# Performance work log

Hardware: AMD Instinct MI355X
Metric: run time of the kernel (lower is better)

## Reference

```python
import jax, jax.numpy as jnp
import numpy as np

N = 50000          # num nodes
E = 800000         # num edges (avg degree 16)
H = 8              # num_heads
CH = [64, 64, 64, 32]  # [in_features] + conv_channels
EPS = 1e-5


def setup_inputs() -> dict:
    key = jax.random.key(0)
    ks = jax.random.split(key, 20)
    x = jax.random.normal(ks[0], (N, CH[0]), jnp.float32)
    src = jax.random.randint(ks[1], (E,), 0, N, dtype=jnp.int32)
    dst = jax.random.randint(ks[2], (E,), 0, N, dtype=jnp.int32)
    dst = jnp.where(src == dst, (dst + 1) % N, dst)  # no self-loops (remove_self_loops)
    edge_index = jnp.stack([src, dst])  # [2, E]

    def lin(k, shape):
        return jax.random.uniform(k, shape, jnp.float32) * 0.1

    inp = {"x": x, "edge_index": edge_index}
    ki = 3
    for layer, (cin, cout) in enumerate(zip(CH[:-1], CH[1:]), start=1):
        inp[f"W{layer}"] = lin(ks[ki], (H * cout, cin)); ki += 1
        inp[f"U{layer}"] = lin(ks[ki], (H, cin)); ki += 1
        inp[f"c{layer}"] = jax.random.normal(ks[ki], (H,), jnp.float32) * 0.1; ki += 1
        inp[f"b{layer}"] = jax.random.normal(ks[ki], (cout,), jnp.float32) * 0.1; ki += 1
        if layer < 3:  # batch norm on intermediate layers only
            inp[f"g{layer}"] = jnp.ones((cout,), jnp.float32)
            inp[f"be{layer}"] = jnp.zeros((cout,), jnp.float32)
    return inp


def _conv(x, src, dst, inv_count, W, U, c, b, out_ch):
    # FeatureSteeredConvolution (translation-invariant attention), mean aggr.
    xi = x[dst]                                   # [E2, Cin] target features
    xj = x[src]                                   # [E2, Cin] source features
    attn = jax.nn.softmax((xi - xj) @ U.T + c, axis=1)   # [E2, H]
    proj = (xj @ W.T).reshape(-1, H, out_ch)      # [E2, H, Cout]
    msg = jnp.einsum('eh,eho->eo', attn, proj)    # [E2, Cout]
    agg = jax.ops.segment_sum(msg, dst, num_segments=N) * inv_count[:, None]
    return agg + b


def _bn(x, g, be):
    # BatchNorm1d, training mode (batch stats, biased variance)
    m = x.mean(axis=0)
    v = ((x - m) ** 2).mean(axis=0)
    return g * (x - m) * jax.lax.rsqrt(v + EPS) + be


def reference(x, edge_index, W1, U1, c1, b1, g1, be1,
              W2, U2, c2, b2, g2, be2, W3, U3, c3, b3):
    loops = jnp.arange(N, dtype=edge_index.dtype)
    src = jnp.concatenate([edge_index[0], loops])  # add_self_loops
    dst = jnp.concatenate([edge_index[1], loops])
    count = jax.ops.segment_sum(jnp.ones_like(dst, jnp.float32), dst, num_segments=N)
    inv_count = 1.0 / count  # every node has its self-loop, so count >= 1

    h = _conv(x, src, dst, inv_count, W1, U1, c1, b1, CH[1])
    h = _bn(jax.nn.relu(h), g1, be1)
    h = _conv(h, src, dst, inv_count, W2, U2, c2, b2, CH[2])
    h = _bn(jax.nn.relu(h), g2, be2)
    return _conv(h, src, dst, inv_count, W3, U3, c3, b3, CH[3])
```

## Files before the change

kernel.cpp:

```cpp
#include <hip/hip_runtime.h>
#include <hip/hip_bf16.h>
#include <hip/hip_fp16.h>
#include <math.h>

constexpr int NN = 50000;
constexpr int NE = 800000;
constexpr float L2E = 1.44269504f;
constexpr int SBLK = 256;
constexpr int SGRID = (NN + SBLK - 1) / SBLK;

typedef __attribute__((ext_vector_type(8))) short bf16x8;
typedef __attribute__((ext_vector_type(4))) float f32x4;

__device__ inline float b2f(unsigned short u) {
  union { unsigned int i; float f; } v;
  v.i = ((unsigned int)u) << 16;
  return v.f;
}

__global__ void k_deg(const int* __restrict__ dst, int* __restrict__ degin) {
  int i = blockIdx.x * blockDim.x + threadIdx.x;
  if (i < NE) atomicAdd(&degin[dst[i]], 1);
}

__global__ void k_inv(const int* __restrict__ degin, float* __restrict__ inv) {
  int i = blockIdx.x * blockDim.x + threadIdx.x;
  if (i < NN) inv[i] = 1.0f / (float)(degin[i] + 1);
}

__global__ void k_scan1(const int* __restrict__ deg, int* __restrict__ bsum) {
  int i = blockIdx.x * SBLK + threadIdx.x;
  int v = (i < NN) ? deg[i] : 0;
#pragma unroll
  for (int off = 32; off; off >>= 1) v += __shfl_down(v, off, 64);
  __shared__ int ws[SBLK / 64];
  if ((threadIdx.x & 63) == 0) ws[threadIdx.x >> 6] = v;
  __syncthreads();
  if (threadIdx.x == 0) {
    int s = 0;
#pragma unroll
    for (int w = 0; w < SBLK / 64; ++w) s += ws[w];
    bsum[blockIdx.x] = s;
  }
}

__global__ void k_scan2(int* __restrict__ bsum) {
  __shared__ int ls[256];
  int t = threadIdx.x;
  int v = (t < SGRID) ? bsum[t] : 0;
  ls[t] = v;
  __syncthreads();
  for (int off = 1; off < 256; off <<= 1) {
    int u = (t >= off) ? ls[t - off] : 0;
    __syncthreads();
    ls[t] += u;
    __syncthreads();
  }
  if (t < SGRID) bsum[t] = ls[t] - v;
}

__global__ void k_scan3(const int* __restrict__ deg, const int* __restrict__ bsum,
                        int* __restrict__ base, int* __restrict__ cursor) {
  __shared__ int ls[SBLK];
  int t = threadIdx.x;
  int i = blockIdx.x * SBLK + t;
  int v = (i < NN) ? deg[i] : 0;
  ls[t] = v;
  __syncthreads();
  for (int off = 1; off < SBLK; off <<= 1) {
    int u = (t >= off) ? ls[t - off] : 0;
    __syncthreads();
    ls[t] += u;
    __syncthreads();
  }
  int ex = ls[t] - v + bsum[blockIdx.x];
  if (i < NN) { base[i] = ex; cursor[i] = ex; }
}

__global__ void k_scatter(const int* __restrict__ src, const int* __restrict__ dst,
                          int* __restrict__ cursor, int* __restrict__ csrc) {
  int e = blockIdx.x * blockDim.x + threadIdx.x;
  if (e < NE) {
    int pos = atomicAdd(&cursor[dst[e]], 1);
    csrc[pos] = src[e];
  }
}

__global__ void k_dstpos(const int* __restrict__ cscbase, const int* __restrict__ degin,
                         int* __restrict__ dstpos) {
  const int lane = threadIdx.x & 63;
  const int n = (int)(((long)blockIdx.x * blockDim.x + threadIdx.x) >> 6);
  if (n >= NN) return;
  const int base = cscbase[n];
  const int end = base + degin[n];
  for (int k = base + lane; k < end; k += 64) dstpos[k] = n;
}

__global__ void k_f2b(const float* __restrict__ in, __hip_bfloat16* __restrict__ out,
                      long n4) {
  long i = (long)blockIdx.x * blockDim.x + threadIdx.x;
  if (i >= n4) return;
  float4 v = reinterpret_cast<const float4*>(in)[i];
  ushort4 o;
  o.x = __hip_bfloat16_raw(__float2bfloat16(v.x)).x;
  o.y = __hip_bfloat16_raw(__float2bfloat16(v.y)).x;
  o.z = __hip_bfloat16_raw(__float2bfloat16(v.z)).x;
  o.w = __hip_bfloat16_raw(__float2bfloat16(v.w)).x;
  reinterpret_cast<ushort4*>(out)[i] = o;
}

__global__ void k_wt(const float* __restrict__ w1, const float* __restrict__ w2,
                     const float* __restrict__ w3, __hip_bfloat16* __restrict__ t1,
                     __hip_bfloat16* __restrict__ t2, __hip_bfloat16* __restrict__ t3) {
  int i = blockIdx.x * blockDim.x + threadIdx.x;
  const int n1 = 64 * 512, n2 = 64 * 512, n3 = 32 * 512;
  const float* w; __hip_bfloat16* t; int cout; int j = i;
  if (j < n1) { w = w1; t = t1; cout = 64; }
  else if ((j -= n1) < n2) { w = w2; t = t2; cout = 64; }
  else if ((j -= n2) < n3) { w = w3; t = t3; cout = 32; }
  else return;
  int o = j >> 9;
  int hc = j & 511;
  int h = hc >> 6, c = hc & 63;
  t[j] = __float2bfloat16(w[(h * cout + o) * 64 + c]);
}

__global__ void k_q(const float* __restrict__ X, const float* __restrict__ U,
                    float* __restrict__ q) {
  int n = blockIdx.x * blockDim.x + threadIdx.x;
  if (n >= NN) return;
  float4 xr[16];
  const float4* X4 = reinterpret_cast<const float4*>(X) + (size_t)n * 16;
#pragma unroll
  for (int i = 0; i < 16; ++i) xr[i] = X4[i];
  const float4* U4 = reinterpret_cast<const float4*>(U);
#pragma unroll
  for (int h = 0; h < 8; ++h) {
    float a = 0.f;
#pragma unroll
    for (int i = 0; i < 16; ++i) {
      float4 u = U4[h * 16 + i];
      a = fmaf(xr[i].x, u.x, a);
      a = fmaf(xr[i].y, u.y, a);
      a = fmaf(xr[i].z, u.z, a);
      a = fmaf(xr[i].w, u.w, a);
    }
    q[(size_t)n * 8 + h] = a * L2E;
  }
}

__global__ void k_attn(const int* __restrict__ csrc, const int* __restrict__ dstpos,
                       const float* __restrict__ q, const float* __restrict__ cvec,
                       const float* __restrict__ inv, uint4* __restrict__ a) {
  int k = blockIdx.x * blockDim.x + threadIdx.x;
  if (k >= NE) return;
  int s = csrc[k], d = dstpos[k];

  const float4* q4 = reinterpret_cast<const float4*>(q);
  const float4* c4 = reinterpret_cast<const float4*>(cvec);
  float4 qd0 = q4[2 * d], qd1 = q4[2 * d + 1];
  float4 qs0 = q4[2 * s], qs1 = q4[2 * s + 1];
  float4 c0 = c4[0], c1 = c4[1];

  float e[8];
  e[0] = __builtin_amdgcn_exp2f(qd0.x - qs0.x + c0.x * L2E);
  e[1] = __builtin_amdgcn_exp2f(qd0.y - qs0.y + c0.y * L2E);
  e[2] = __builtin_amdgcn_exp2f(qd0.z - qs0.z + c0.z * L2E);
  e[3] = __builtin_amdgcn_exp2f(qd0.w - qs0.w + c0.w * L2E);
  e[4] = __builtin_amdgcn_exp2f(qd1.x - qs1.x + c1.x * L2E);
  e[5] = __builtin_amdgcn_exp2f(qd1.y - qs1.y + c1.y * L2E);
  e[6] = __builtin_amdgcn_exp2f(qd1.z - qs1.z + c1.z * L2E);
  e[7] = __builtin_amdgcn_exp2f(qd1.w - qs1.w + c1.w * L2E);

  float sum = ((e[0] + e[1]) + (e[2] + e[3])) + ((e[4] + e[5]) + (e[6] + e[7]));
  float r = __builtin_amdgcn_rcpf(sum) * inv[d];

  __half2 h0 = __floats2half2_rn(e[0] * r, e[1] * r);
  __half2 h1 = __floats2half2_rn(e[2] * r, e[3] * r);
  __half2 h2 = __floats2half2_rn(e[4] * r, e[5] * r);
  __half2 h3 = __floats2half2_rn(e[6] * r, e[7] * r);
  uint4 o;
  o.x = *(unsigned int*)&h0;
  o.y = *(unsigned int*)&h1;
  o.z = *(unsigned int*)&h2;
  o.w = *(unsigned int*)&h3;
  a[k] = o;
}

#define ZACC(AV, XS)                                                      \
  do {                                                                    \
    float2 f0 = __half22float2(*(__half2*)&(AV).x);                       \
    float2 f1 = __half22float2(*(__half2*)&(AV).y);                       \
    float2 f2 = __half22float2(*(__half2*)&(AV).z);                       \
    float2 f3 = __half22float2(*(__half2*)&(AV).w);                       \
    z[0] = fmaf(f0.x, (XS), z[0]);                                        \
    z[1] = fmaf(f0.y, (XS), z[1]);                                        \
    z[2] = fmaf(f1.x, (XS), z[2]);                                        \
    z[3] = fmaf(f1.y, (XS), z[3]);                                        \
    z[4] = fmaf(f2.x, (XS), z[4]);                                        \
    z[5] = fmaf(f2.y, (XS), z[5]);                                        \
    z[6] = fmaf(f3.x, (XS), z[6]);                                        \
    z[7] = fmaf(f3.y, (XS), z[7]);                                        \
  } while (0)

__global__ void k_zagg(const int* __restrict__ cscbase, const int* __restrict__ cscend,
                       const int* __restrict__ csrc, const uint4* __restrict__ a,
                       const ushort* __restrict__ xb, const float* __restrict__ inv,
                       const float* __restrict__ cvec, __hip_bfloat16* __restrict__ zb) {
  const int lane = threadIdx.x & 63;
  const int n = (int)(((long)blockIdx.x * blockDim.x + threadIdx.x) >> 6);
  if (n >= NN) return;

  float wc[8], wsum = 0.f;
#pragma unroll
  for (int h = 0; h < 8; ++h) { wc[h] = __builtin_amdgcn_exp2f(cvec[h] * L2E); wsum += wc[h]; }
  const float rxd = __builtin_amdgcn_rcpf(wsum) * inv[n] * b2f(xb[(size_t)n * 64 + lane]);
  float z[8];
#pragma unroll
  for (int h = 0; h < 8; ++h) z[h] = wc[h] * rxd;

  int k = cscbase[n];
  const int k1 = cscend[n];
  for (; k + 4 <= k1; k += 4) {
    int s0 = csrc[k + 0];
    int s1 = csrc[k + 1];
    int s2 = csrc[k + 2];
    int s3 = csrc[k + 3];
    uint4 a0 = a[k + 0];
    uint4 a1 = a[k + 1];
    uint4 a2 = a[k + 2];
    uint4 a3 = a[k + 3];
    float x0 = b2f(xb[(size_t)s0 * 64 + lane]);
    float x1 = b2f(xb[(size_t)s1 * 64 + lane]);
    float x2 = b2f(xb[(size_t)s2 * 64 + lane]);
    float x3 = b2f(xb[(size_t)s3 * 64 + lane]);
    ZACC(a0, x0);
    ZACC(a1, x1);
    ZACC(a2, x2);
    ZACC(a3, x3);
  }
  for (; k < k1; ++k) {
    int s = csrc[k];
    uint4 av = a[k];
    float xs = b2f(xb[(size_t)s * 64 + lane]);
    ZACC(av, xs);
  }

  ushort* zo = reinterpret_cast<ushort*>(zb) + (size_t)n * 512 + lane;
#pragma unroll
  for (int h = 0; h < 8; ++h)
    zo[h * 64] = __hip_bfloat16_raw(__float2bfloat16(z[h])).x;
}

template <int JOUT, bool RS>
__global__ void __launch_bounds__(256)
k_zgemm_ep(const __hip_bfloat16* __restrict__ Zb, const __hip_bfloat16* __restrict__ Wt,
           const float* __restrict__ b, float* __restrict__ yout,
           float* __restrict__ stats) {
  __shared__ float ssum[64], ssq[64];
  const int lane = threadIdx.x & 63;
  const int w = threadIdx.x >> 6;
  const int m0 = (blockIdx.x * 4 + w) * 64;
  const int lr = lane & 15;
  const int lk = lane >> 4;
  constexpr int NT = JOUT / 16;

  if (RS && threadIdx.x < 64) { ssum[threadIdx.x] = 0.f; ssq[threadIdx.x] = 0.f; }
  if (RS) __syncthreads();

  const ushort* Z = reinterpret_cast<const ushort*>(Zb);
  const ushort* W = reinterpret_cast<const ushort*>(Wt);

  f32x4 acc[4][NT] = {};
  for (int kk = 0; kk < 16; ++kk) {
    bf16x8 bfr[NT];
#pragma unroll
    for (int ni = 0; ni < NT; ++ni) {
      int j = ni * 16 + lr;
      bfr[ni] = *reinterpret_cast<const bf16x8*>(W + (size_t)j * 512 + kk * 32 + lk * 8);
    }
#pragma unroll
    for (int mi = 0; mi < 4; ++mi) {
      int r = m0 + mi * 16 + lr;
      if (r >= NN) r = NN - 1;
      bf16x8 afr = *reinterpret_cast<const bf16x8*>(Z + (size_t)r * 512 + kk * 32 + lk * 8);
#pragma unroll
      for (int ni = 0; ni < NT; ++ni)
        acc[mi][ni] = __builtin_amdgcn_mfma_f32_16x16x32_bf16(afr, bfr[ni], acc[mi][ni], 0, 0, 0);
    }
  }

  float bj[NT];
#pragma unroll
  for (int ni = 0; ni < NT; ++ni) bj[ni] = b[ni * 16 + lr];

  float ps[NT] = {}, pq[NT] = {};
#pragma unroll
  for (int mi = 0; mi < 4; ++mi) {
#pragma unroll
    for (int i = 0; i < 4; ++i) {
      int r = m0 + mi * 16 + lk * 4 + i;
      if (r < NN) {
#pragma unroll
        for (int ni = 0; ni < NT; ++ni) {
          float v = acc[mi][ni][i] + bj[ni];
          if (RS) {
            v = fmaxf(v, 0.f);
            ps[ni] += v;
            pq[ni] = fmaf(v, v, pq[ni]);
          }
          yout[(size_t)r * JOUT + ni * 16 + lr] = v;
        }
      }
    }
  }

  if (RS) {
#pragma unroll
    for (int ni = 0; ni < NT; ++ni) {
      atomicAdd(&ssum[ni * 16 + lr], ps[ni]);
      atomicAdd(&ssq[ni * 16 + lr], pq[ni]);
    }
    __syncthreads();
    if (threadIdx.x < 64) {
      atomicAdd(&stats[threadIdx.x], ssum[threadIdx.x]);
      atomicAdd(&stats[64 + threadIdx.x], ssq[threadIdx.x]);
    }
  }
}

__global__ void __launch_bounds__(256)
k_bnq(const float* __restrict__ y, const float* __restrict__ stats,
      const float* __restrict__ g, const float* __restrict__ be,
      const float* __restrict__ U, __hip_bfloat16* __restrict__ xb,
      float* __restrict__ q) {
  const int lane = threadIdx.x & 63;
  const int n = (int)(((long)blockIdx.x * blockDim.x + threadIdx.x) >> 6);
  if (n >= NN) return;

  float m = stats[lane] * (1.0f / NN);
  float v = stats[64 + lane] * (1.0f / NN) - m * m;
  float r = fmaf(g[lane] * rsqrtf(v + 1e-5f), y[(size_t)n * 64 + lane] - m, be[lane]);
  xb[(size_t)n * 64 + lane] = __float2bfloat16(r);

  float qv[8];
#pragma unroll
  for (int h = 0; h < 8; ++h) {
    float p = r * U[h * 64 + lane];
#pragma unroll
    for (int off = 32; off; off >>= 1) p += __shfl_xor(p, off, 64);
    qv[h] = p;
  }
  if (lane == 0) {
    float4* q4 = reinterpret_cast<float4*>(q + (size_t)n * 8);
    q4[0] = make_float4(qv[0] * L2E, qv[1] * L2E, qv[2] * L2E, qv[3] * L2E);
    q4[1] = make_float4(qv[4] * L2E, qv[5] * L2E, qv[6] * L2E, qv[7] * L2E);
  }
}

extern "C" void kernel_launch(void* const* d_in, const int* in_sizes, int n_in,
                              void* d_out, int out_size, void* d_ws, size_t ws_size,
                              hipStream_t stream) {
  const float* x   = (const float*)d_in[0];
  const int*   src = (const int*)d_in[1];
  const int*   dst = src + NE;
  const float* W1 = (const float*)d_in[2];
  const float* U1 = (const float*)d_in[3];
  const float* c1 = (const float*)d_in[4];
  const float* b1 = (const float*)d_in[5];
  const float* g1 = (const float*)d_in[6];
  const float* be1 = (const float*)d_in[7];
  const float* W2 = (const float*)d_in[8];
  const float* U2 = (const float*)d_in[9];
  const float* c2 = (const float*)d_in[10];
  const float* b2 = (const float*)d_in[11];
  const float* g2 = (const float*)d_in[12];
  const float* be2 = (const float*)d_in[13];
  const float* W3 = (const float*)d_in[14];
  const float* U3 = (const float*)d_in[15];
  const float* c3 = (const float*)d_in[16];
  const float* b3 = (const float*)d_in[17];
  float* out = (float*)d_out;

  float* ws   = (float*)d_ws;
  float* inv  = ws;
  float* q    = inv + NN;
  float* y    = q + (size_t)NN * 8;
  float* stats = y + (size_t)NN * 64;
  uint4* a    = (uint4*)(stats + 128);
  __hip_bfloat16* xb = (__hip_bfloat16*)(a + NE);
  __hip_bfloat16* zb = xb + (size_t)NN * 64;
  __hip_bfloat16* Wt1 = zb + (size_t)NN * 512;
  __hip_bfloat16* Wt2 = Wt1 + 64 * 512;
  __hip_bfloat16* Wt3 = Wt2 + 64 * 512;
  int* degin   = (int*)(Wt3 + 32 * 512);
  int* cscbase = degin + NN;
  int* cursor  = cscbase + NN;
  int* bsum    = cursor + NN;
  int* csrc    = bsum + 256;
  int* dstpos  = csrc + NE;

  const int BLK = 256;
  dim3 b256(BLK);

  hipMemsetAsync(degin, 0, (size_t)NN * 4, stream);
  k_deg<<<dim3((NE + BLK - 1) / BLK), b256, 0, stream>>>(dst, degin);
  k_inv<<<dim3((NN + BLK - 1) / BLK), b256, 0, stream>>>(degin, inv);
  k_scan1<<<dim3(SGRID), dim3(SBLK), 0, stream>>>(degin, bsum);
  k_scan2<<<dim3(1), dim3(256), 0, stream>>>(bsum);
  k_scan3<<<dim3(SGRID), dim3(SBLK), 0, stream>>>(degin, bsum, cscbase, cursor);
  k_scatter<<<dim3((NE + BLK - 1) / BLK), b256, 0, stream>>>(src, dst, cursor, csrc);
  k_dstpos<<<dim3(NN * 64 / BLK), b256, 0, stream>>>(cscbase, degin, dstpos);

  const int qgrid = (NN + BLK - 1) / BLK;
  const int attn_grid = (NE + BLK - 1) / BLK;
  const int node_grid = NN * 64 / BLK;
  const int zgemm_grid = (NN + 255) / 256;
  const long xb4 = (long)NN * 64 / 4;
  const int wtgrid = (64 * 512 * 2 + 32 * 512 + BLK - 1) / BLK;

  k_f2b<<<dim3((xb4 + BLK - 1) / BLK), b256, 0, stream>>>(x, xb, xb4);
  k_wt<<<dim3(wtgrid), b256, 0, stream>>>(W1, W2, W3, Wt1, Wt2, Wt3);

  k_q<<<dim3(qgrid), b256, 0, stream>>>(x, U1, q);
  k_attn<<<dim3(attn_grid), b256, 0, stream>>>(csrc, dstpos, q, c1, inv, a);
  k_zagg<<<dim3(node_grid), b256, 0, stream>>>(cscbase, cursor, csrc, a,
                                               (const ushort*)xb, inv, c1, zb);
  hipMemsetAsync(stats, 0, 128 * 4, stream);
  k_zgemm_ep<64, true><<<dim3(zgemm_grid), b256, 0, stream>>>(zb, Wt1, b1, y, stats);
  k_bnq<<<dim3(node_grid), b256, 0, stream>>>(y, stats, g1, be1, U2, xb, q);

  k_attn<<<dim3(attn_grid), b256, 0, stream>>>(csrc, dstpos, q, c2, inv, a);
  k_zagg<<<dim3(node_grid), b256, 0, stream>>>(cscbase, cursor, csrc, a,
                                               (const ushort*)xb, inv, c2, zb);
  hipMemsetAsync(stats, 0, 128 * 4, stream);
  k_zgemm_ep<64, true><<<dim3(zgemm_grid), b256, 0, stream>>>(zb, Wt2, b2, y, stats);
  k_bnq<<<dim3(node_grid), b256, 0, stream>>>(y, stats, g2, be2, U3, xb, q);

  k_attn<<<dim3(attn_grid), b256, 0, stream>>>(csrc, dstpos, q, c3, inv, a);
  k_zagg<<<dim3(node_grid), b256, 0, stream>>>(cscbase, cursor, csrc, a,
                                               (const ushort*)xb, inv, c3, zb);
  k_zgemm_ep<32, false><<<dim3(zgemm_grid), b256, 0, stream>>>(zb, Wt3, b3, out, nullptr);
}
```

Before: 419.7 us.

## Fuse edge attention into aggregation, slice CSR scatter, store BN input as bf16

Removes the separate per-edge attention kernel and its fp16 attention buffer. k_zagg now computes the softmax weights on the fly, with 8 edges per wave and 8 heads per edge, and distributes them through wave shuffles. It also drops the dstpos kernel and array, makes the CSR scatter slice destinations by block group for better atomic locality, and writes the intermediate pre-BN activations as bf16 instead of fp32. These changes cut memory traffic and kernel launches, but they add shuffle overhead and a partially idle tail loop in aggregation, plus a small loss of precision in the intermediate activations.

```diff
diff --git a/kernel.cpp b/kernel.cpp
--- a/kernel.cpp
+++ b/kernel.cpp
@@ -8,6 +8,8 @@
 constexpr float L2E = 1.44269504f;
 constexpr int SBLK = 256;
 constexpr int SGRID = (NN + SBLK - 1) / SBLK;
+constexpr int NSLICE = 8;
+constexpr int DPS = (NN + NSLICE - 1) / NSLICE;
 
 typedef __attribute__((ext_vector_type(8))) short bf16x8;
 typedef __attribute__((ext_vector_type(4))) float f32x4;
@@ -79,21 +81,17 @@
 
 __global__ void k_scatter(const int* __restrict__ src, const int* __restrict__ dst,
                           int* __restrict__ cursor, int* __restrict__ csrc) {
-  int e = blockIdx.x * blockDim.x + threadIdx.x;
-  if (e < NE) {
-    int pos = atomicAdd(&cursor[dst[e]], 1);
-    csrc[pos] = src[e];
-  }
-}
-
-__global__ void k_dstpos(const int* __restrict__ cscbase, const int* __restrict__ degin,
-                         int* __restrict__ dstpos) {
-  const int lane = threadIdx.x & 63;
-  const int n = (int)(((long)blockIdx.x * blockDim.x + threadIdx.x) >> 6);
-  if (n >= NN) return;
-  const int base = cscbase[n];
-  const int end = base + degin[n];
-  for (int k = base + lane; k < end; k += 64) dstpos[k] = n;
+  const int slice = blockIdx.x & (NSLICE - 1);
+  const int chunk = blockIdx.x >> 3;
+  const int nchunks = gridDim.x >> 3;
+  for (int e = chunk * blockDim.x + threadIdx.x; e < NE;
+       e += nchunks * blockDim.x) {
+    int d = dst[e];
+    if (d / DPS == slice) {
+      int pos = atomicAdd(&cursor[d], 1);
+      csrc[pos] = src[e];
+    }
+  }
 }
 
 __global__ void k_f2b(const float* __restrict__ in, __hip_bfloat16* __restrict__ out,
@@ -149,114 +147,84 @@
   }
 }
 
-__global__ void k_attn(const int* __restrict__ csrc, const int* __restrict__ dstpos,
-                       const float* __restrict__ q, const float* __restrict__ cvec,
-                       const float* __restrict__ inv, uint4* __restrict__ a) {
-  int k = blockIdx.x * blockDim.x + threadIdx.x;
-  if (k >= NE) return;
-  int s = csrc[k], d = dstpos[k];
-
-  const float4* q4 = reinterpret_cast<const float4*>(q);
-  const float4* c4 = reinterpret_cast<const float4*>(cvec);
-  float4 qd0 = q4[2 * d], qd1 = q4[2 * d + 1];
-  float4 qs0 = q4[2 * s], qs1 = q4[2 * s + 1];
-  float4 c0 = c4[0], c1 = c4[1];
-
-  float e[8];
-  e[0] = __builtin_amdgcn_exp2f(qd0.x - qs0.x + c0.x * L2E);
-  e[1] = __builtin_amdgcn_exp2f(qd0.y - qs0.y + c0.y * L2E);
-  e[2] = __builtin_amdgcn_exp2f(qd0.z - qs0.z + c0.z * L2E);
-  e[3] = __builtin_amdgcn_exp2f(qd0.w - qs0.w + c0.w * L2E);
-  e[4] = __builtin_amdgcn_exp2f(qd1.x - qs1.x + c1.x * L2E);
-  e[5] = __builtin_amdgcn_exp2f(qd1.y - qs1.y + c1.y * L2E);
-  e[6] = __builtin_amdgcn_exp2f(qd1.z - qs1.z + c1.z * L2E);
-  e[7] = __builtin_amdgcn_exp2f(qd1.w - qs1.w + c1.w * L2E);
-
-  float sum = ((e[0] + e[1]) + (e[2] + e[3])) + ((e[4] + e[5]) + (e[6] + e[7]));
-  float r = __builtin_amdgcn_rcpf(sum) * inv[d];
-
-  __half2 h0 = __floats2half2_rn(e[0] * r, e[1] * r);
-  __half2 h1 = __floats2half2_rn(e[2] * r, e[3] * r);
-  __half2 h2 = __floats2half2_rn(e[4] * r, e[5] * r);
-  __half2 h3 = __floats2half2_rn(e[6] * r, e[7] * r);
-  uint4 o;
-  o.x = *(unsigned int*)&h0;
-  o.y = *(unsigned int*)&h1;
-  o.z = *(unsigned int*)&h2;
-  o.w = *(unsigned int*)&h3;
-  a[k] = o;
-}
-
-#define ZACC(AV, XS)                                                      \
-  do {                                                                    \
-    float2 f0 = __half22float2(*(__half2*)&(AV).x);                       \
-    float2 f1 = __half22float2(*(__half2*)&(AV).y);                       \
-    float2 f2 = __half22float2(*(__half2*)&(AV).z);                       \
-    float2 f3 = __half22float2(*(__half2*)&(AV).w);                       \
-    z[0] = fmaf(f0.x, (XS), z[0]);                                        \
-    z[1] = fmaf(f0.y, (XS), z[1]);                                        \
-    z[2] = fmaf(f1.x, (XS), z[2]);                                        \
-    z[3] = fmaf(f1.y, (XS), z[3]);                                        \
-    z[4] = fmaf(f2.x, (XS), z[4]);                                        \
-    z[5] = fmaf(f2.y, (XS), z[5]);                                        \
-    z[6] = fmaf(f3.x, (XS), z[6]);                                        \
-    z[7] = fmaf(f3.y, (XS), z[7]);                                        \
-  } while (0)
-
 __global__ void k_zagg(const int* __restrict__ cscbase, const int* __restrict__ cscend,
-                       const int* __restrict__ csrc, const uint4* __restrict__ a,
+                       const int* __restrict__ csrc, const float* __restrict__ q,
                        const ushort* __restrict__ xb, const float* __restrict__ inv,
                        const float* __restrict__ cvec, __hip_bfloat16* __restrict__ zb) {
   const int lane = threadIdx.x & 63;
   const int n = (int)(((long)blockIdx.x * blockDim.x + threadIdx.x) >> 6);
   if (n >= NN) return;
+  const int h = lane & 7;
+
+  const float tbh = q[(size_t)n * 8 + h] + cvec[h] * L2E;
 
   float wc[8], wsum = 0.f;
 #pragma unroll
-  for (int h = 0; h < 8; ++h) { wc[h] = __builtin_amdgcn_exp2f(cvec[h] * L2E); wsum += wc[h]; }
-  const float rxd = __builtin_amdgcn_rcpf(wsum) * inv[n] * b2f(xb[(size_t)n * 64 + lane]);
+  for (int hh = 0; hh < 8; ++hh) {
+    wc[hh] = __builtin_amdgcn_exp2f(cvec[hh] * L2E);
+    wsum += wc[hh];
+  }
+  const float rxd = __builtin_amdgcn_rcpf(wsum) * b2f(xb[(size_t)n * 64 + lane]);
   float z[8];
 #pragma unroll
-  for (int h = 0; h < 8; ++h) z[h] = wc[h] * rxd;
+  for (int hh = 0; hh < 8; ++hh) z[hh] = wc[hh] * rxd;
 
   int k = cscbase[n];
   const int k1 = cscend[n];
-  for (; k + 4 <= k1; k += 4) {
-    int s0 = csrc[k + 0];
-    int s1 = csrc[k + 1];
-    int s2 = csrc[k + 2];
-    int s3 = csrc[k + 3];
-    uint4 a0 = a[k + 0];
-    uint4 a1 = a[k + 1];
-    uint4 a2 = a[k + 2];
-    uint4 a3 = a[k + 3];
-    float x0 = b2f(xb[(size_t)s0 * 64 + lane]);
-    float x1 = b2f(xb[(size_t)s1 * 64 + lane]);
-    float x2 = b2f(xb[(size_t)s2 * 64 + lane]);
-    float x3 = b2f(xb[(size_t)s3 * 64 + lane]);
-    ZACC(a0, x0);
-    ZACC(a1, x1);
-    ZACC(a2, x2);
-    ZACC(a3, x3);
-  }
-  for (; k < k1; ++k) {
-    int s = csrc[k];
-    uint4 av = a[k];
-    float xs = b2f(xb[(size_t)s * 64 + lane]);
-    ZACC(av, xs);
-  }
-
+  while (k < k1) {
+    const int rem = k1 - k;
+    const int nv = rem < 8 ? rem : 8;
+    int myk = k + (lane >> 3);
+    if (myk > k1 - 1) myk = k1 - 1;
+    const int sm = csrc[myk];
+
+    const float e = __builtin_amdgcn_exp2f(tbh - q[(size_t)sm * 8 + h]);
+    float sum = e;
+    sum += __shfl_xor(sum, 1, 64);
+    sum += __shfl_xor(sum, 2, 64);
+    sum += __shfl_xor(sum, 4, 64);
+    const float am = e * __builtin_amdgcn_rcpf(sum);
+
+    float xv[8];
+#pragma unroll
+    for (int t = 0; t < 8; ++t) {
+      int st = __shfl(sm, t * 8, 64);
+      xv[t] = b2f(xb[(size_t)st * 64 + lane]);
+    }
+    for (int t = 0; t < nv; ++t) {
+      const int bl = t * 8;
+      float a0 = __shfl(am, bl + 0, 64);
+      float a1 = __shfl(am, bl + 1, 64);
+      float a2 = __shfl(am, bl + 2, 64);
+      float a3 = __shfl(am, bl + 3, 64);
+      float a4 = __shfl(am, bl + 4, 64);
+      float a5 = __shfl(am, bl + 5, 64);
+      float a6 = __shfl(am, bl + 6, 64);
+      float a7 = __shfl(am, bl + 7, 64);
+      z[0] = fmaf(a0, xv[t], z[0]);
+      z[1] = fmaf(a1, xv[t], z[1]);
+      z[2] = fmaf(a2, xv[t], z[2]);
+      z[3] = fmaf(a3, xv[t], z[3]);
+      z[4] = fmaf(a4, xv[t], z[4]);
+      z[5] = fmaf(a5, xv[t], z[5]);
+      z[6] = fmaf(a6, xv[t], z[6]);
+      z[7] = fmaf(a7, xv[t], z[7]);
+    }
+    k += 8;
+  }
+
+  const float sc = inv[n];
   ushort* zo = reinterpret_cast<ushort*>(zb) + (size_t)n * 512 + lane;
 #pragma unroll
-  for (int h = 0; h < 8; ++h)
-    zo[h * 64] = __hip_bfloat16_raw(__float2bfloat16(z[h])).x;
+  for (int hh = 0; hh < 8; ++hh)
+    zo[hh * 64] = __hip_bfloat16_raw(__float2bfloat16(z[hh] * sc)).x;
 }
 
 template <int JOUT, bool RS>
 __global__ void __launch_bounds__(256)
 k_zgemm_ep(const __hip_bfloat16* __restrict__ Zb, const __hip_bfloat16* __restrict__ Wt,
-           const float* __restrict__ b, float* __restrict__ yout,
-           float* __restrict__ stats) {
+           const float* __restrict__ b, __hip_bfloat16* __restrict__ yb,
+           float* __restrict__ fout, float* __restrict__ stats) {
   __shared__ float ssum[64], ssq[64];
   const int lane = threadIdx.x & 63;
   const int w = threadIdx.x >> 6;
@@ -308,8 +276,10 @@
             v = fmaxf(v, 0.f);
             ps[ni] += v;
             pq[ni] = fmaf(v, v, pq[ni]);
+            yb[(size_t)r * JOUT + ni * 16 + lr] = __float2bfloat16(v);
+          } else {
+            fout[(size_t)r * JOUT + ni * 16 + lr] = v;
           }
-          yout[(size_t)r * JOUT + ni * 16 + lr] = v;
         }
       }
     }
@@ -330,7 +300,7 @@
 }
 
 __global__ void __launch_bounds__(256)
-k_bnq(const float* __restrict__ y, const float* __restrict__ stats,
+k_bnq(const __hip_bfloat16* __restrict__ y, const float* __restrict__ stats,
       const float* __restrict__ g, const float* __restrict__ be,
       const float* __restrict__ U, __hip_bfloat16* __restrict__ xb,
       float* __restrict__ q) {
@@ -340,7 +310,8 @@
 
   float m = stats[lane] * (1.0f / NN);
   float v = stats[64 + lane] * (1.0f / NN) - m * m;
-  float r = fmaf(g[lane] * rsqrtf(v + 1e-5f), y[(size_t)n * 64 + lane] - m, be[lane]);
+  float yv = b2f(reinterpret_cast<const ushort*>(y)[(size_t)n * 64 + lane]);
+  float r = fmaf(g[lane] * rsqrtf(v + 1e-5f), yv - m, be[lane]);
   xb[(size_t)n * 64 + lane] = __float2bfloat16(r);
 
   float qv[8];
@@ -385,10 +356,9 @@
   float* ws   = (float*)d_ws;
   float* inv  = ws;
   float* q    = inv + NN;
-  float* y    = q + (size_t)NN * 8;
-  float* stats = y + (size_t)NN * 64;
-  uint4* a    = (uint4*)(stats + 128);
-  __hip_bfloat16* xb = (__hip_bfloat16*)(a + NE);
+  float* stats = q + (size_t)NN * 8;
+  __hip_bfloat16* yb = (__hip_bfloat16*)(stats + 128);
+  __hip_bfloat16* xb = yb + (size_t)NN * 64;
   __hip_bfloat16* zb = xb + (size_t)NN * 64;
   __hip_bfloat16* Wt1 = zb + (size_t)NN * 512;
   __hip_bfloat16* Wt2 = Wt1 + 64 * 512;
@@ -398,7 +368,6 @@
   int* cursor  = cscbase + NN;
   int* bsum    = cursor + NN;
   int* csrc    = bsum + 256;
-  int* dstpos  = csrc + NE;
 
   const int BLK = 256;
   dim3 b256(BLK);
@@ -409,11 +378,9 @@
   k_scan1<<<dim3(SGRID), dim3(SBLK), 0, stream>>>(degin, bsum);
   k_scan2<<<dim3(1), dim3(256), 0, stream>>>(bsum);
   k_scan3<<<dim3(SGRID), dim3(SBLK), 0, stream>>>(degin, bsum, cscbase, cursor);
-  k_scatter<<<dim3((NE + BLK - 1) / BLK), b256, 0, stream>>>(src, dst, cursor, csrc);
-  k_dstpos<<<dim3(NN * 64 / BLK), b256, 0, stream>>>(cscbase, degin, dstpos);
+  k_scatter<<<dim3(8 * 104), b256, 0, stream>>>(src, dst, cursor, csrc);
 
   const int qgrid = (NN + BLK - 1) / BLK;
-  const int attn_grid = (NE + BLK - 1) / BLK;
   const int node_grid = NN * 64 / BLK;
   const int zgemm_grid = (NN + 255) / 256;
   const long xb4 = (long)NN * 64 / 4;
@@ -423,22 +390,19 @@
   k_wt<<<dim3(wtgrid), b256, 0, stream>>>(W1, W2, W3, Wt1, Wt2, Wt3);
 
   k_q<<<dim3(qgrid), b256, 0, stream>>>(x, U1, q);
-  k_attn<<<dim3(attn_grid), b256, 0, stream>>>(csrc, dstpos, q, c1, inv, a);
-  k_zagg<<<dim3(node_grid), b256, 0, stream>>>(cscbase, cursor, csrc, a,
+  k_zagg<<<dim3(node_grid), b256, 0, stream>>>(cscbase, cursor, csrc, q,
                                                (const ushort*)xb, inv, c1, zb);
   hipMemsetAsync(stats, 0, 128 * 4, stream);
-  k_zgemm_ep<64, true><<<dim3(zgemm_grid), b256, 0, stream>>>(zb, Wt1, b1, y, stats);
-  k_bnq<<<dim3(node_grid), b256, 0, stream>>>(y, stats, g1, be1, U2, xb, q);
-
-  k_attn<<<dim3(attn_grid), b256, 0, stream>>>(csrc, dstpos, q, c2, inv, a);
-  k_zagg<<<dim3(node_grid), b256, 0, stream>>>(cscbase, cursor, csrc, a,
+  k_zgemm_ep<64, true><<<dim3(zgemm_grid), b256, 0, stream>>>(zb, Wt1, b1, yb, nullptr, stats);
+  k_bnq<<<dim3(node_grid), b256, 0, stream>>>(yb, stats, g1, be1, U2, xb, q);
+
+  k_zagg<<<dim3(node_grid), b256, 0, stream>>>(cscbase, cursor, csrc, q,
                                                (const ushort*)xb, inv, c2, zb);
   hipMemsetAsync(stats, 0, 128 * 4, stream);
-  k_zgemm_ep<64, true><<<dim3(zgemm_grid), b256, 0, stream>>>(zb, Wt2, b2, y, stats);
-  k_bnq<<<dim3(node_grid), b256, 0, stream>>>(y, stats, g2, be2, U3, xb, q);
-
-  k_attn<<<dim3(attn_grid), b256, 0, stream>>>(csrc, dstpos, q, c3, inv, a);
-  k_zagg<<<dim3(node_grid), b256, 0, stream>>>(cscbase, cursor, csrc, a,
+  k_zgemm_ep<64, true><<<dim3(zgemm_grid), b256, 0, stream>>>(zb, Wt2, b2, yb, nullptr, stats);
+  k_bnq<<<dim3(node_grid), b256, 0, stream>>>(yb, stats, g2, be2, U3, xb, q);
+
+  k_zagg<<<dim3(node_grid), b256, 0, stream>>>(cscbase, cursor, csrc, q,
                                                (const ushort*)xb, inv, c3, zb);
-  k_zgemm_ep<32, false><<<dim3(zgemm_grid), b256, 0, stream>>>(zb, Wt3, b3, out, nullptr);
-}
+  k_zgemm_ep<32, false><<<dim3(zgemm_grid), b256, 0, stream>>>(zb, Wt3, b3, nullptr, out, nullptr);
+}
```

New measurement: 502.5 us. 1.2x slower.

## Slice CSR scatter by destination range and store intermediate activations in bf16

Applied to the files above, without the earlier changes.

The CSR scatter kernel now launches 8 slices of blocks. Each slice scans every edge but only inserts the ones whose destination falls in its node range, so the atomics and csrc writes land in a more localized region. The intermediate post-ReLU activations between the GEMM epilogue and the batch-norm kernel are now stored as bf16 instead of fp32, which halves that write and read traffic. In exchange, each edge's dst is read 8 times, and the pre-BN values lose precision, although BN statistics are still accumulated in fp32.

```diff
diff --git a/kernel.cpp b/kernel.cpp
--- a/kernel.cpp
+++ b/kernel.cpp
@@ -8,6 +8,8 @@
 constexpr float L2E = 1.44269504f;
 constexpr int SBLK = 256;
 constexpr int SGRID = (NN + SBLK - 1) / SBLK;
+constexpr int NSLICE = 8;
+constexpr int DPS = (NN + NSLICE - 1) / NSLICE;
 
 typedef __attribute__((ext_vector_type(8))) short bf16x8;
 typedef __attribute__((ext_vector_type(4))) float f32x4;
@@ -79,10 +81,16 @@
 
 __global__ void k_scatter(const int* __restrict__ src, const int* __restrict__ dst,
                           int* __restrict__ cursor, int* __restrict__ csrc) {
-  int e = blockIdx.x * blockDim.x + threadIdx.x;
-  if (e < NE) {
-    int pos = atomicAdd(&cursor[dst[e]], 1);
-    csrc[pos] = src[e];
+  const int slice = blockIdx.x & (NSLICE - 1);
+  const int chunk = blockIdx.x >> 3;
+  const int nchunks = gridDim.x >> 3;
+  for (int e = chunk * blockDim.x + threadIdx.x; e < NE;
+       e += nchunks * blockDim.x) {
+    int d = dst[e];
+    if (d / DPS == slice) {
+      int pos = atomicAdd(&cursor[d], 1);
+      csrc[pos] = src[e];
+    }
   }
 }
 
@@ -255,8 +263,8 @@
 template <int JOUT, bool RS>
 __global__ void __launch_bounds__(256)
 k_zgemm_ep(const __hip_bfloat16* __restrict__ Zb, const __hip_bfloat16* __restrict__ Wt,
-           const float* __restrict__ b, float* __restrict__ yout,
-           float* __restrict__ stats) {
+           const float* __restrict__ b, __hip_bfloat16* __restrict__ yb,
+           float* __restrict__ fout, float* __restrict__ stats) {
   __shared__ float ssum[64], ssq[64];
   const int lane = threadIdx.x & 63;
   const int w = threadIdx.x >> 6;
@@ -308,8 +316,10 @@
             v = fmaxf(v, 0.f);
             ps[ni] += v;
             pq[ni] = fmaf(v, v, pq[ni]);
+            yb[(size_t)r * JOUT + ni * 16 + lr] = __float2bfloat16(v);
+          } else {
+            fout[(size_t)r * JOUT + ni * 16 + lr] = v;
           }
-          yout[(size_t)r * JOUT + ni * 16 + lr] = v;
         }
       }
     }
@@ -330,7 +340,7 @@
 }
 
 __global__ void __launch_bounds__(256)
-k_bnq(const float* __restrict__ y, const float* __restrict__ stats,
+k_bnq(const __hip_bfloat16* __restrict__ y, const float* __restrict__ stats,
       const float* __restrict__ g, const float* __restrict__ be,
       const float* __restrict__ U, __hip_bfloat16* __restrict__ xb,
       float* __restrict__ q) {
@@ -340,7 +350,8 @@
 
   float m = stats[lane] * (1.0f / NN);
   float v = stats[64 + lane] * (1.0f / NN) - m * m;
-  float r = fmaf(g[lane] * rsqrtf(v + 1e-5f), y[(size_t)n * 64 + lane] - m, be[lane]);
+  float yv = b2f(reinterpret_cast<const ushort*>(y)[(size_t)n * 64 + lane]);
+  float r = fmaf(g[lane] * rsqrtf(v + 1e-5f), yv - m, be[lane]);
   xb[(size_t)n * 64 + lane] = __float2bfloat16(r);
 
   float qv[8];
@@ -385,10 +396,10 @@
   float* ws   = (float*)d_ws;
   float* inv  = ws;
   float* q    = inv + NN;
-  float* y    = q + (size_t)NN * 8;
-  float* stats = y + (size_t)NN * 64;
+  float* stats = q + (size_t)NN * 8;
   uint4* a    = (uint4*)(stats + 128);
-  __hip_bfloat16* xb = (__hip_bfloat16*)(a + NE);
+  __hip_bfloat16* yb = (__hip_bfloat16*)(a + NE);
+  __hip_bfloat16* xb = yb + (size_t)NN * 64;
   __hip_bfloat16* zb = xb + (size_t)NN * 64;
   __hip_bfloat16* Wt1 = zb + (size_t)NN * 512;
   __hip_bfloat16* Wt2 = Wt1 + 64 * 512;
@@ -409,7 +420,7 @@
   k_scan1<<<dim3(SGRID), dim3(SBLK), 0, stream>>>(degin, bsum);
   k_scan2<<<dim3(1), dim3(256), 0, stream>>>(bsum);
   k_scan3<<<dim3(SGRID), dim3(SBLK), 0, stream>>>(degin, bsum, cscbase, cursor);
-  k_scatter<<<dim3((NE + BLK - 1) / BLK), b256, 0, stream>>>(src, dst, cursor, csrc);
+  k_scatter<<<dim3(8 * 104), b256, 0, stream>>>(src, dst, cursor, csrc);
   k_dstpos<<<dim3(NN * 64 / BLK), b256, 0, stream>>>(cscbase, degin, dstpos);
 
   const int qgrid = (NN + BLK - 1) / BLK;
@@ -427,18 +438,18 @@
   k_zagg<<<dim3(node_grid), b256, 0, stream>>>(cscbase, cursor, csrc, a,
                                                (const ushort*)xb, inv, c1, zb);
   hipMemsetAsync(stats, 0, 128 * 4, stream);
-  k_zgemm_ep<64, true><<<dim3(zgemm_grid), b256, 0, stream>>>(zb, Wt1, b1, y, stats);
-  k_bnq<<<dim3(node_grid), b256, 0, stream>>>(y, stats, g1, be1, U2, xb, q);
+  k_zgemm_ep<64, true><<<dim3(zgemm_grid), b256, 0, stream>>>(zb, Wt1, b1, yb, nullptr, stats);
+  k_bnq<<<dim3(node_grid), b256, 0, stream>>>(yb, stats, g1, be1, U2, xb, q);
 
   k_attn<<<dim3(attn_grid), b256, 0, stream>>>(csrc, dstpos, q, c2, inv, a);
   k_zagg<<<dim3(node_grid), b256, 0, stream>>>(cscbase, cursor, csrc, a,
                                                (const ushort*)xb, inv, c2, zb);
   hipMemsetAsync(stats, 0, 128 * 4, stream);
-  k_zgemm_ep<64, true><<<dim3(zgemm_grid), b256, 0, stream>>>(zb, Wt2, b2, y, stats);
-  k_bnq<<<dim3(node_grid), b256, 0, stream>>>(y, stats, g2, be2, U3, xb, q);
+  k_zgemm_ep<64, true><<<dim3(zgemm_grid), b256, 0, stream>>>(zb, Wt2, b2, yb, nullptr, stats);
+  k_bnq<<<dim3(node_grid), b256, 0, stream>>>(yb, stats, g2, be2, U3, xb, q);
 
   k_attn<<<dim3(attn_grid), b256, 0, stream>>>(csrc, dstpos, q, c3, inv, a);
   k_zagg<<<dim3(node_grid), b256, 0, stream>>>(cscbase, cursor, csrc, a,
                                                (const ushort*)xb, inv, c3, zb);
-  k_zgemm_ep<32, false><<<dim3(zgemm_grid), b256, 0, stream>>>(zb, Wt3, b3, out, nullptr);
-}
+  k_zgemm_ep<32, false><<<dim3(zgemm_grid), b256, 0, stream>>>(zb, Wt3, b3, nullptr, out, nullptr);
+}
```

Measured after the change: 411.8 us. About the same (-1.9%).
